# Optimization experiments

Measured on AMD Instinct MI355X. Metric: run time of the kernel, lower is better.

Reference implementation:

```python
import jax, jax.numpy as jnp
import numpy as np

N, F, M, B = 100000, 256, 10, 32768
DECAY = 0.9


def setup_inputs() -> dict:
    key = jax.random.key(0)
    ks = jax.random.split(key, 16)
    s = 1.0 / np.sqrt(F)
    # forward args
    node_indices = jax.random.permutation(ks[0], N)[:B]  # unique indices
    node_features = jax.random.normal(ks[1], (B, F), jnp.float32)
    # per-node state
    hidden_states = jax.random.normal(ks[2], (N, F), jnp.float32) * 0.1
    cell_states = jax.random.normal(ks[3], (N, F), jnp.float32) * 0.1
    temporal_memory = jax.random.normal(ks[4], (N, M, F), jnp.float32) * 0.1
    memory_ptr = jax.random.randint(ks[5], (N,), 0, M)
    # LSTMCell params (gate order i, f, g, o as in torch)
    W_ih = jax.random.normal(ks[6], (4 * F, F), jnp.float32) * s
    W_hh = jax.random.normal(ks[7], (4 * F, F), jnp.float32) * s
    b_ih = jax.random.normal(ks[8], (4 * F,), jnp.float32) * s
    b_hh = jax.random.normal(ks[9], (4 * F,), jnp.float32) * s
    # attention read params
    Wq = jax.random.normal(ks[10], (F, F), jnp.float32) * s
    bq = jnp.zeros((F,), jnp.float32)
    Wk = jax.random.normal(ks[11], (F, F), jnp.float32) * s
    bk = jnp.zeros((F,), jnp.float32)
    Wv = jax.random.normal(ks[12], (F, F), jnp.float32) * s
    bv = jnp.zeros((F,), jnp.float32)
    return dict(node_indices=node_indices, node_features=node_features,
                hidden_states=hidden_states, cell_states=cell_states,
                temporal_memory=temporal_memory, memory_ptr=memory_ptr,
                W_ih=W_ih, W_hh=W_hh, b_ih=b_ih, b_hh=b_hh,
                Wq=Wq, bq=bq, Wk=Wk, bk=bk, Wv=Wv, bv=bv)


def reference(node_indices, node_features, hidden_states, cell_states,
              temporal_memory, memory_ptr, W_ih, W_hh, b_ih, b_hh,
              Wq, bq, Wk, bk, Wv, bv):
    idx = node_indices
    feat = node_features.shape[-1]
    # --- update_memory: LSTMCell on gathered per-node states ---
    h_prev = hidden_states[idx]              # (B, F)
    c_prev = cell_states[idx]                # (B, F)
    gates = node_features @ W_ih.T + b_ih + h_prev @ W_hh.T + b_hh
    i, f, g, o = jnp.split(gates, 4, axis=-1)
    c_new = jax.nn.sigmoid(f) * c_prev + jax.nn.sigmoid(i) * jnp.tanh(g)
    h_new = jax.nn.sigmoid(o) * jnp.tanh(c_new)
    # --- scatter into circular temporal memory + decay previous slot ---
    ptr = memory_ptr[idx]                    # (B,)
    tm = temporal_memory.at[idx, ptr].set(node_features)
    prev = ptr - 1                           # -1 wraps; decay only applied if ptr > 0
    old = tm[idx, prev]                      # (B, F)
    tm = tm.at[idx, prev].set(jnp.where((ptr > 0)[:, None], old * DECAY, old))
    # --- get_temporal_context: gather + tiny attention over M slots ---
    mem = tm[idx]                            # (B, M, F)
    q = h_new @ Wq.T + bq                    # (B, F)  hidden_states[idx] post-update == h_new
    k = mem @ Wk.T + bk                      # (B, M, F)
    v = mem @ Wv.T + bv                      # (B, M, F)
    scores = jnp.einsum('bf,bmf->bm', q, k) / jnp.sqrt(jnp.asarray(feat, q.dtype))
    w = jax.nn.softmax(scores, axis=-1)      # (B, M)
    context = jnp.einsum('bmf,bm->bf', v, w) # (B, F)
    return context
```

## Files before the change

kernel.cpp:

```cpp
#include <hip/hip_runtime.h>
#include <hip/hip_bf16.h>

constexpr int NB = 32768;
constexpr int NF = 256;
constexpr int NM = 10;
constexpr float DECAY = 0.9f;

using bf16x8 = __attribute__((ext_vector_type(8))) short;
using f32x4  = __attribute__((ext_vector_type(4))) float;

static __device__ __forceinline__ ushort f2bf(float x) {
    unsigned u = __float_as_uint(x);
    unsigned r = (u + 0x7fffu + ((u >> 16) & 1u)) >> 16;
    return (ushort)r;
}
static __device__ __forceinline__ float bf2f(ushort x) {
    return __uint_as_float(((unsigned)x) << 16);
}
static __device__ __forceinline__ float sigmoid_f(float x) {
    return 1.f / (1.f + __expf(-x));
}
static __device__ __forceinline__ float tanh_f(float x) {
    float e = __expf(2.f * x);
    return (e - 1.f) / (e + 1.f);
}
static __device__ __forceinline__ void gload16(const void* g, void* l) {
    __builtin_amdgcn_global_load_lds(
        (const __attribute__((address_space(1))) unsigned int*)g,
        (__attribute__((address_space(3))) unsigned int*)l, 16, 0, 0);
}

constexpr int PB_ACAT = 16384;
constexpr int PB_WGI  = PB_ACAT + 1024;
constexpr int PB_WQKT = PB_WGI + 256;
constexpr int PB_WV   = PB_WQKT + 256;
constexpr int PB_TOT  = PB_WV + 1;

__global__ __launch_bounds__(256) void k_prep(
    const float* __restrict__ W_ih, const float* __restrict__ W_hh,
    const float* __restrict__ b_ih, const float* __restrict__ b_hh,
    const float* __restrict__ Wq, const float* __restrict__ bq,
    const float* __restrict__ Wk, const float* __restrict__ Wv,
    const float* __restrict__ nf, const float* __restrict__ hidden,
    const int* __restrict__ idx,
    ushort* __restrict__ Wgi, float* __restrict__ bsum,
    ushort* __restrict__ WqkT, float* __restrict__ bqk,
    ushort* __restrict__ Wvb, ushort* __restrict__ Acat)
{
    const int blk = blockIdx.x, tid = threadIdx.x;
    if (blk < PB_ACAT) {
        int t = blk * 256 + tid;
        int row = t >> 7;
        int c4 = (t & 127) * 4;
        const float* src = (c4 < 256) ? (nf + (size_t)row * 256 + c4)
                                      : (hidden + (size_t)idx[row] * 256 + (c4 - 256));
        float4 v = *reinterpret_cast<const float4*>(src);
        ushort4 o;
        o.x = f2bf(v.x); o.y = f2bf(v.y); o.z = f2bf(v.z); o.w = f2bf(v.w);
        *reinterpret_cast<ushort4*>(Acat + (size_t)row * 512 + c4) = o;
    } else if (blk < PB_WGI) {
        int j = blk - PB_ACAT;
        int f = j >> 2, g = j & 3;
        int sr = g * 256 + f;
        for (int c = tid; c < 512; c += 256) {
            float v = (c < 256) ? W_ih[sr * 256 + c] : W_hh[sr * 256 + (c - 256)];
            Wgi[j * 512 + c] = f2bf(v);
        }
        if (tid == 0) bsum[j] = b_ih[sr] + b_hh[sr];
    } else if (blk < PB_WQKT) {
        int i = blk - PB_WGI, a = tid;
        float s = 0.f;
#pragma unroll 8
        for (int j = 0; j < 256; ++j) s += Wq[j * 256 + a] * Wk[j * 256 + i];
        WqkT[i * 256 + a] = f2bf(s * 0.0625f);
    } else if (blk < PB_WV) {
        int t = (blk - PB_WQKT) * 256 + tid;
        Wvb[t] = f2bf(Wv[t]);
    } else {
        int i = tid;
        float s = 0.f;
#pragma unroll 8
        for (int j = 0; j < 256; ++j) s += bq[j] * Wk[j * 256 + i];
        bqk[i] = s * 0.0625f;
    }
}

__global__ __launch_bounds__(256) void k_gates2(
    const ushort* __restrict__ Acat, const ushort* __restrict__ Wgi,
    const float* __restrict__ bsum, const int* __restrict__ idx,
    const float* __restrict__ cell, ushort* __restrict__ h_new)
{
    __shared__ ushort As[128 * 32];
    __shared__ ushort Bs[128 * 32];
    const int t = threadIdx.x;
    const int w = t >> 6, l = t & 63;
    const int wr = w >> 1, wc = w & 1;
    const int lr = l & 15, lk = l >> 4;
    const int row0 = blockIdx.x * 128;
    const int col0 = blockIdx.y * 128;

    f32x4 acc[4][4];
#pragma unroll
    for (int m = 0; m < 4; ++m)
#pragma unroll
        for (int n = 0; n < 4; ++n) acc[m][n] = f32x4{0.f, 0.f, 0.f, 0.f};

    const int srow = l >> 2;
    const int scol = (l & 3) * 8;
    const int u0 = w * 2, u1 = u0 + 1;
    const ushort* aS0 = Acat + (size_t)(row0 + u0 * 16 + srow) * 512 + scol;
    const ushort* aS1 = Acat + (size_t)(row0 + u1 * 16 + srow) * 512 + scol;
    const ushort* bS0 = Wgi  + (size_t)(col0 + u0 * 16 + srow) * 512 + scol;
    const ushort* bS1 = Wgi  + (size_t)(col0 + u1 * 16 + srow) * 512 + scol;
    ushort* aL0 = As + u0 * 512; ushort* aL1 = As + u1 * 512;
    ushort* bL0 = Bs + u0 * 512; ushort* bL1 = Bs + u1 * 512;

    for (int k0 = 0; k0 < 512; k0 += 32) {
        gload16(aS0 + k0, aL0);
        gload16(aS1 + k0, aL1);
        gload16(bS0 + k0, bL0);
        gload16(bS1 + k0, bL1);
        __syncthreads();
        bf16x8 af[4], bfr[4];
#pragma unroll
        for (int m = 0; m < 4; ++m)
            af[m] = *reinterpret_cast<const bf16x8*>(As + (wr * 64 + m * 16 + lr) * 32 + lk * 8);
#pragma unroll
        for (int n = 0; n < 4; ++n)
            bfr[n] = *reinterpret_cast<const bf16x8*>(Bs + (wc * 64 + n * 16 + lr) * 32 + lk * 8);
#pragma unroll
        for (int m = 0; m < 4; ++m)
#pragma unroll
            for (int n = 0; n < 4; ++n)
                acc[m][n] = __builtin_amdgcn_mfma_f32_16x16x32_bf16(af[m], bfr[n], acc[m][n], 0, 0, 0);
        __syncthreads();
    }

    float bb[4];
#pragma unroll
    for (int n = 0; n < 4; ++n) bb[n] = bsum[col0 + wc * 64 + n * 16 + lr];
#pragma unroll
    for (int m = 0; m < 4; ++m)
#pragma unroll
        for (int n = 0; n < 4; ++n)
#pragma unroll
            for (int r = 0; r < 4; ++r) acc[m][n][r] += bb[n];

    const int g0 = lr & 3;
    const int fq = lr >> 2;
    const bool is0 = (g0 == 0), is1 = (g0 == 1), is2 = (g0 == 2), is3 = (g0 == 3);
    const int fbase = (col0 >> 2) + wc * 16;

    int nodev[4];
#pragma unroll
    for (int r = 0; r < 4; ++r)
        nodev[r] = idx[row0 + wr * 64 + g0 * 16 + lk * 4 + r];

#pragma unroll
    for (int n = 0; n < 4; ++n) {
#pragma unroll
        for (int r = 0; r < 4; ++r) {
            float own = is0 ? acc[0][n][r] : is1 ? acc[1][n][r] : is2 ? acc[2][n][r] : acc[3][n][r];
            float s1  = is0 ? acc[1][n][r] : is1 ? acc[0][n][r] : is2 ? acc[3][n][r] : acc[2][n][r];
            float s2  = is0 ? acc[2][n][r] : is1 ? acc[3][n][r] : is2 ? acc[0][n][r] : acc[1][n][r];
            float s3  = is0 ? acc[3][n][r] : is1 ? acc[2][n][r] : is2 ? acc[1][n][r] : acc[0][n][r];
            float r1 = __shfl_xor(s1, 1, 64);
            float r2 = __shfl_xor(s2, 2, 64);
            float r3 = __shfl_xor(s3, 3, 64);
            float gi = is0 ? own : is1 ? r1 : is2 ? r2 : r3;
            float gf = is1 ? own : is0 ? r1 : is3 ? r2 : r3;
            float gg = is2 ? own : is3 ? r1 : is0 ? r2 : r3;
            float go = is3 ? own : is2 ? r1 : is1 ? r2 : r3;
            int fg = fbase + n * 4 + fq;
            float cp = cell[(size_t)nodev[r] * 256 + fg];
            float cn = sigmoid_f(gf) * cp + sigmoid_f(gi) * tanh_f(gg);
            float hn = sigmoid_f(go) * tanh_f(cn);
            int grow = row0 + wr * 64 + g0 * 16 + lk * 4 + r;
            h_new[(size_t)grow * 256 + fg] = f2bf(hn);
        }
    }
}

static __device__ __forceinline__ int swzb(int row, int byteInRow) {
    return (row * 512 + byteInRow) ^ ((row & 7) << 4);
}

__global__ __launch_bounds__(256) void k_tail(
    const ushort* __restrict__ hnew, const ushort* __restrict__ WqkT,
    const float* __restrict__ bqk, const ushort* __restrict__ Wvb,
    const float* __restrict__ bv,
    const int* __restrict__ idx, const int* __restrict__ mptr,
    const float* __restrict__ tm, const float* __restrict__ nf,
    float* __restrict__ out)
{
    __shared__ ushort sQ[32 * 256];
    const int t = threadIdx.x, w = t >> 6, l = t & 63;
    const int lr = l & 15, lk = l >> 4;
    const int row0 = blockIdx.x * 32;
    char* sB = (char*)sQ;

    f32x4 acc[2][4];
#pragma unroll
    for (int m = 0; m < 2; ++m)
#pragma unroll
        for (int n = 0; n < 4; ++n) acc[m][n] = f32x4{0.f, 0.f, 0.f, 0.f};

    const ushort* aptr[2];
#pragma unroll
    for (int m = 0; m < 2; ++m) aptr[m] = hnew + (size_t)(row0 + m * 16 + lr) * 256 + lk * 8;
    const ushort* bptr[4];
#pragma unroll
    for (int n = 0; n < 4; ++n) bptr[n] = WqkT + (size_t)(w * 64 + n * 16 + lr) * 256 + lk * 8;

#pragma unroll 2
    for (int k = 0; k < 256; k += 32) {
        bf16x8 a[2], b[4];
#pragma unroll
        for (int m = 0; m < 2; ++m) a[m] = *reinterpret_cast<const bf16x8*>(aptr[m] + k);
#pragma unroll
        for (int n = 0; n < 4; ++n) b[n] = *reinterpret_cast<const bf16x8*>(bptr[n] + k);
#pragma unroll
        for (int m = 0; m < 2; ++m)
#pragma unroll
            for (int n = 0; n < 4; ++n)
                acc[m][n] = __builtin_amdgcn_mfma_f32_16x16x32_bf16(a[m], b[n], acc[m][n], 0, 0, 0);
    }
#pragma unroll
    for (int m = 0; m < 2; ++m)
#pragma unroll
        for (int n = 0; n < 4; ++n) {
            int colc = w * 64 + n * 16 + lr;
            float bbq = bqk[colc];
#pragma unroll
            for (int r = 0; r < 4; ++r) {
                int row = m * 16 + lk * 4 + r;
                *(ushort*)(sB + swzb(row, colc * 2)) = f2bf(acc[m][n][r] + bbq);
            }
        }
    __syncthreads();

    {
        const int b0 = row0 + w * 8;
        int nodes[8], ptrs[8];
#pragma unroll
        for (int r = 0; r < 8; ++r) { nodes[r] = idx[b0 + r]; ptrs[r] = mptr[nodes[r]]; }

#pragma unroll 2
        for (int rr = 0; rr < 8; ++rr) {
            int row = w * 8 + rr;
            int b = b0 + rr;
            int node = nodes[rr];
            int ptr = ptrs[rr];
            ushort4 q4 = *(const ushort4*)(sB + swzb(row, l * 8));
            float q0 = bf2f(q4.x), q1 = bf2f(q4.y), q2 = bf2f(q4.z), q3 = bf2f(q4.w);
            const float* base = tm + (size_t)node * (NM * NF);

            float4 mem[NM];
            float sc[NM];
#pragma unroll
            for (int m = 0; m < NM; ++m) {
                float4 v;
                if (m == ptr) {
                    v = *reinterpret_cast<const float4*>(nf + (size_t)b * 256 + l * 4);
                } else {
                    v = *reinterpret_cast<const float4*>(base + (size_t)m * 256 + l * 4);
                    if (ptr > 0 && m == ptr - 1) { v.x *= DECAY; v.y *= DECAY; v.z *= DECAY; v.w *= DECAY; }
                }
                mem[m] = v;
                sc[m] = q0 * v.x + q1 * v.y + q2 * v.z + q3 * v.w;
            }
#pragma unroll
            for (int m = 0; m < NM; ++m) {
                float s = sc[m];
#pragma unroll
                for (int d = 1; d < 64; d <<= 1) s += __shfl_xor(s, d, 64);
                sc[m] = s;
            }
            float mx = sc[0];
#pragma unroll
            for (int m = 1; m < NM; ++m) mx = fmaxf(mx, sc[m]);
            float e[NM], sum = 0.f;
#pragma unroll
            for (int m = 0; m < NM; ++m) { e[m] = __expf(sc[m] - mx); sum += e[m]; }
            float inv = 1.f / sum;

            float4 c = {0.f, 0.f, 0.f, 0.f};
#pragma unroll
            for (int m = 0; m < NM; ++m) {
                float wm = e[m] * inv;
                c.x += wm * mem[m].x; c.y += wm * mem[m].y; c.z += wm * mem[m].z; c.w += wm * mem[m].w;
            }
            ushort4 o;
            o.x = f2bf(c.x); o.y = f2bf(c.y); o.z = f2bf(c.z); o.w = f2bf(c.w);
            *(ushort4*)(sB + swzb(row, l * 8)) = o;
        }
    }
    __syncthreads();

#pragma unroll
    for (int m = 0; m < 2; ++m)
#pragma unroll
        for (int n = 0; n < 4; ++n) acc[m][n] = f32x4{0.f, 0.f, 0.f, 0.f};
    const ushort* vptr[4];
#pragma unroll
    for (int n = 0; n < 4; ++n) vptr[n] = Wvb + (size_t)(w * 64 + n * 16 + lr) * 256 + lk * 8;

#pragma unroll 2
    for (int k = 0; k < 256; k += 32) {
        bf16x8 a[2], b[4];
#pragma unroll
        for (int m = 0; m < 2; ++m)
            a[m] = *reinterpret_cast<const bf16x8*>(sB + swzb(m * 16 + lr, (k + lk * 8) * 2));
#pragma unroll
        for (int n = 0; n < 4; ++n) b[n] = *reinterpret_cast<const bf16x8*>(vptr[n] + k);
#pragma unroll
        for (int m = 0; m < 2; ++m)
#pragma unroll
            for (int n = 0; n < 4; ++n)
                acc[m][n] = __builtin_amdgcn_mfma_f32_16x16x32_bf16(a[m], b[n], acc[m][n], 0, 0, 0);
    }
#pragma unroll
    for (int m = 0; m < 2; ++m)
#pragma unroll
        for (int n = 0; n < 4; ++n) {
            int colc = w * 64 + n * 16 + lr;
            float bbv = bv[colc];
#pragma unroll
            for (int r = 0; r < 4; ++r) {
                int row = m * 16 + lk * 4 + r;
                out[(size_t)(row0 + row) * 256 + colc] = acc[m][n][r] + bbv;
            }
        }
}

extern "C" void kernel_launch(void* const* d_in, const int* in_sizes, int n_in,
                              void* d_out, int out_size, void* d_ws, size_t ws_size,
                              hipStream_t stream) {
    const int*   node_indices = (const int*)  d_in[0];
    const float* node_feats   = (const float*)d_in[1];
    const float* hidden       = (const float*)d_in[2];
    const float* cell         = (const float*)d_in[3];
    const float* tmem         = (const float*)d_in[4];
    const int*   memory_ptr   = (const int*)  d_in[5];
    const float* W_ih         = (const float*)d_in[6];
    const float* W_hh         = (const float*)d_in[7];
    const float* b_ih         = (const float*)d_in[8];
    const float* b_hh         = (const float*)d_in[9];
    const float* Wq           = (const float*)d_in[10];
    const float* bq           = (const float*)d_in[11];
    const float* Wk           = (const float*)d_in[12];
    const float* Wv           = (const float*)d_in[14];
    const float* bv           = (const float*)d_in[15];

    char* ws = (char*)d_ws;
    size_t off = 0;
    auto alloc = [&](size_t bytes) { char* p = ws + off; off += (bytes + 255) & ~(size_t)255; return p; };

    ushort* Wgi   = (ushort*)alloc((size_t)1024 * 512 * 2);
    ushort* WqkT  = (ushort*)alloc((size_t)256 * 256 * 2);
    ushort* Wvb   = (ushort*)alloc((size_t)256 * 256 * 2);
    float*  bqk   = (float*) alloc((size_t)256 * 4);
    float*  bsum  = (float*) alloc((size_t)1024 * 4);
    ushort* Acat  = (ushort*)alloc((size_t)NB * 512 * 2);
    ushort* hnew  = (ushort*)alloc((size_t)NB * 256 * 2);

    k_prep<<<PB_TOT, 256, 0, stream>>>(W_ih, W_hh, b_ih, b_hh, Wq, bq, Wk, Wv,
                                       node_feats, hidden, node_indices,
                                       Wgi, bsum, WqkT, bqk, Wvb, Acat);
    k_gates2<<<dim3(NB / 128, 8), 256, 0, stream>>>(Acat, Wgi, bsum, node_indices, cell, hnew);
    k_tail<<<NB / 32, 256, 0, stream>>>(hnew, WqkT, bqk, Wvb, bv,
                                        node_indices, memory_ptr, tmem, node_feats,
                                        (float*)d_out);
}
```

Measured before the change: 223.5 us.

## Split tail kernel into q-projection GEMM and attention+output kernel

The fused tail kernel is split in two. The first kernel computes the q/k projection with 64-row tiles and stages the A operand through LDS, writing q to a new workspace buffer. The second kernel runs the attention over memory slots and the Wv GEMM with 16-row blocks, which launches more blocks for the gather-bound phase. The aim is better occupancy and parallelism during the gather of temporal memory, at the cost of an extra launch and an extra round trip of q through global memory.

Result: faster. 218.8 us (-2.1%).

```diff
diff --git a/kernel.cpp b/kernel.cpp
--- a/kernel.cpp
+++ b/kernel.cpp
@@ -181,73 +181,95 @@
     }
 }
 
-static __device__ __forceinline__ int swzb(int row, int byteInRow) {
-    return (row * 512 + byteInRow) ^ ((row & 7) << 4);
-}
-
-__global__ __launch_bounds__(256) void k_tail(
+__global__ __launch_bounds__(256) void k_qk(
     const ushort* __restrict__ hnew, const ushort* __restrict__ WqkT,
-    const float* __restrict__ bqk, const ushort* __restrict__ Wvb,
-    const float* __restrict__ bv,
-    const int* __restrict__ idx, const int* __restrict__ mptr,
-    const float* __restrict__ tm, const float* __restrict__ nf,
-    float* __restrict__ out)
+    const float* __restrict__ bqk, ushort* __restrict__ qbuf)
 {
-    __shared__ ushort sQ[32 * 256];
+    __shared__ ushort As[64 * 32];
     const int t = threadIdx.x, w = t >> 6, l = t & 63;
     const int lr = l & 15, lk = l >> 4;
-    const int row0 = blockIdx.x * 32;
-    char* sB = (char*)sQ;
-
-    f32x4 acc[2][4];
-#pragma unroll
-    for (int m = 0; m < 2; ++m)
+    const int row0 = blockIdx.x * 64;
+
+    f32x4 acc[4][4];
+#pragma unroll
+    for (int m = 0; m < 4; ++m)
 #pragma unroll
         for (int n = 0; n < 4; ++n) acc[m][n] = f32x4{0.f, 0.f, 0.f, 0.f};
 
-    const ushort* aptr[2];
-#pragma unroll
-    for (int m = 0; m < 2; ++m) aptr[m] = hnew + (size_t)(row0 + m * 16 + lr) * 256 + lk * 8;
+    const int srow = w * 16 + (l >> 2);
+    const int scol = (l & 3) * 8;
+    const ushort* aS = hnew + (size_t)(row0 + srow) * 256 + scol;
+    ushort* aL = As + (w * 16) * 32;
+
     const ushort* bptr[4];
 #pragma unroll
     for (int n = 0; n < 4; ++n) bptr[n] = WqkT + (size_t)(w * 64 + n * 16 + lr) * 256 + lk * 8;
 
-#pragma unroll 2
-    for (int k = 0; k < 256; k += 32) {
-        bf16x8 a[2], b[4];
-#pragma unroll
-        for (int m = 0; m < 2; ++m) a[m] = *reinterpret_cast<const bf16x8*>(aptr[m] + k);
-#pragma unroll
-        for (int n = 0; n < 4; ++n) b[n] = *reinterpret_cast<const bf16x8*>(bptr[n] + k);
-#pragma unroll
-        for (int m = 0; m < 2; ++m)
+    for (int k0 = 0; k0 < 256; k0 += 32) {
+        gload16(aS + k0, aL);
+        __syncthreads();
+        bf16x8 a[4], b[4];
+#pragma unroll
+        for (int m = 0; m < 4; ++m)
+            a[m] = *reinterpret_cast<const bf16x8*>(As + (m * 16 + lr) * 32 + lk * 8);
+#pragma unroll
+        for (int n = 0; n < 4; ++n) b[n] = *reinterpret_cast<const bf16x8*>(bptr[n] + k0);
+#pragma unroll
+        for (int m = 0; m < 4; ++m)
 #pragma unroll
             for (int n = 0; n < 4; ++n)
                 acc[m][n] = __builtin_amdgcn_mfma_f32_16x16x32_bf16(a[m], b[n], acc[m][n], 0, 0, 0);
-    }
-#pragma unroll
-    for (int m = 0; m < 2; ++m)
+        __syncthreads();
+    }
+
+#pragma unroll
+    for (int m = 0; m < 4; ++m)
 #pragma unroll
         for (int n = 0; n < 4; ++n) {
             int colc = w * 64 + n * 16 + lr;
             float bbq = bqk[colc];
 #pragma unroll
             for (int r = 0; r < 4; ++r) {
-                int row = m * 16 + lk * 4 + r;
-                *(ushort*)(sB + swzb(row, colc * 2)) = f2bf(acc[m][n][r] + bbq);
+                int row = row0 + m * 16 + lk * 4 + r;
+                qbuf[(size_t)row * 256 + colc] = f2bf(acc[m][n][r] + bbq);
             }
         }
+}
+
+static __device__ __forceinline__ int swzb(int row, int byteInRow) {
+    return (row * 512 + byteInRow) ^ ((row & 7) << 4);
+}
+
+__global__ __launch_bounds__(256) void k_attnout(
+    const ushort* __restrict__ qbuf, const ushort* __restrict__ Wvb,
+    const float* __restrict__ bv, const int* __restrict__ idx,
+    const int* __restrict__ mptr, const float* __restrict__ tm,
+    const float* __restrict__ nf, float* __restrict__ out)
+{
+    __shared__ ushort sQ[16 * 256];
+    char* sB = (char*)sQ;
+    const int t = threadIdx.x, w = t >> 6, l = t & 63;
+    const int lr = l & 15, lk = l >> 4;
+    const int row0 = blockIdx.x * 16;
+
+#pragma unroll
+    for (int ch = t; ch < 512; ch += 256) {
+        int row = ch >> 5;
+        int pos = (ch & 31) * 16;
+        *reinterpret_cast<uint4*>(sB + swzb(row, pos)) =
+            *reinterpret_cast<const uint4*>((const char*)(qbuf + (size_t)(row0 + row) * 256) + pos);
+    }
     __syncthreads();
 
     {
-        const int b0 = row0 + w * 8;
-        int nodes[8], ptrs[8];
-#pragma unroll
-        for (int r = 0; r < 8; ++r) { nodes[r] = idx[b0 + r]; ptrs[r] = mptr[nodes[r]]; }
-
-#pragma unroll 2
-        for (int rr = 0; rr < 8; ++rr) {
-            int row = w * 8 + rr;
+        const int b0 = row0 + w * 4;
+        int nodes[4], ptrs[4];
+#pragma unroll
+        for (int r = 0; r < 4; ++r) { nodes[r] = idx[b0 + r]; ptrs[r] = mptr[nodes[r]]; }
+
+#pragma unroll
+        for (int rr = 0; rr < 4; ++rr) {
+            int row = w * 4 + rr;
             int b = b0 + rr;
             int node = nodes[rr];
             int ptr = ptrs[rr];
@@ -297,40 +319,33 @@
     }
     __syncthreads();
 
-#pragma unroll
-    for (int m = 0; m < 2; ++m)
-#pragma unroll
-        for (int n = 0; n < 4; ++n) acc[m][n] = f32x4{0.f, 0.f, 0.f, 0.f};
+    f32x4 acc[4];
+#pragma unroll
+    for (int n = 0; n < 4; ++n) acc[n] = f32x4{0.f, 0.f, 0.f, 0.f};
     const ushort* vptr[4];
 #pragma unroll
     for (int n = 0; n < 4; ++n) vptr[n] = Wvb + (size_t)(w * 64 + n * 16 + lr) * 256 + lk * 8;
 
 #pragma unroll 2
     for (int k = 0; k < 256; k += 32) {
-        bf16x8 a[2], b[4];
-#pragma unroll
-        for (int m = 0; m < 2; ++m)
-            a[m] = *reinterpret_cast<const bf16x8*>(sB + swzb(m * 16 + lr, (k + lk * 8) * 2));
+        bf16x8 a = *reinterpret_cast<const bf16x8*>(sB + swzb(lr, (k + lk * 8) * 2));
+        bf16x8 b[4];
 #pragma unroll
         for (int n = 0; n < 4; ++n) b[n] = *reinterpret_cast<const bf16x8*>(vptr[n] + k);
 #pragma unroll
-        for (int m = 0; m < 2; ++m)
-#pragma unroll
-            for (int n = 0; n < 4; ++n)
-                acc[m][n] = __builtin_amdgcn_mfma_f32_16x16x32_bf16(a[m], b[n], acc[m][n], 0, 0, 0);
-    }
-#pragma unroll
-    for (int m = 0; m < 2; ++m)
-#pragma unroll
-        for (int n = 0; n < 4; ++n) {
-            int colc = w * 64 + n * 16 + lr;
-            float bbv = bv[colc];
-#pragma unroll
-            for (int r = 0; r < 4; ++r) {
-                int row = m * 16 + lk * 4 + r;
-                out[(size_t)(row0 + row) * 256 + colc] = acc[m][n][r] + bbv;
-            }
-        }
+        for (int n = 0; n < 4; ++n)
+            acc[n] = __builtin_amdgcn_mfma_f32_16x16x32_bf16(a, b[n], acc[n], 0, 0, 0);
+    }
+#pragma unroll
+    for (int n = 0; n < 4; ++n) {
+        int colc = w * 64 + n * 16 + lr;
+        float bbv = bv[colc];
+#pragma unroll
+        for (int r = 0; r < 4; ++r) {
+            int row = lk * 4 + r;
+            out[(size_t)(row0 + row) * 256 + colc] = acc[n][r] + bbv;
+        }
+    }
 }
 
 extern "C" void kernel_launch(void* const* d_in, const int* in_sizes, int n_in,
@@ -363,12 +378,13 @@
     float*  bsum  = (float*) alloc((size_t)1024 * 4);
     ushort* Acat  = (ushort*)alloc((size_t)NB * 512 * 2);
     ushort* hnew  = (ushort*)alloc((size_t)NB * 256 * 2);
+    ushort* qbuf  = (ushort*)alloc((size_t)NB * 256 * 2);
 
     k_prep<<<PB_TOT, 256, 0, stream>>>(W_ih, W_hh, b_ih, b_hh, Wq, bq, Wk, Wv,
                                        node_feats, hidden, node_indices,
                                        Wgi, bsum, WqkT, bqk, Wvb, Acat);
     k_gates2<<<dim3(NB / 128, 8), 256, 0, stream>>>(Acat, Wgi, bsum, node_indices, cell, hnew);
-    k_tail<<<NB / 32, 256, 0, stream>>>(hnew, WqkT, bqk, Wvb, bv,
-                                        node_indices, memory_ptr, tmem, node_feats,
-                                        (float*)d_out);
-}
+    k_qk<<<NB / 64, 256, 0, stream>>>(hnew, WqkT, bqk, qbuf);
+    k_attnout<<<NB / 16, 256, 0, stream>>>(qbuf, Wvb, bv, node_indices, memory_ptr,
+                                           tmem, node_feats, (float*)d_out);
+}
```
